# Kernel tuning notes

Hardware: AMD Instinct MI355X
Metric: run time of the kernel (lower is better)

Reference implementation:

```python
import jax, jax.numpy as jnp
import numpy as np

HIDDEN = 96
INF = 1e30


def setup_inputs() -> dict:
    key = jax.random.key(0)
    ks = jax.random.split(key, 9)
    B, JX, JM, D_IN, D_MEM = 8, 2048, 2048, 150, 150
    GATED = D_IN + D_MEM  # 300
    inputs = jax.random.normal(ks[0], (B, JX, D_IN), dtype=jnp.float32)
    memory = jax.random.normal(ks[1], (B, JM, D_MEM), dtype=jnp.float32)
    mask = jax.random.randint(ks[2], (B, JM), 0, 2, dtype=jnp.int32)
    s_in = 1.0 / np.sqrt(D_IN)
    s_g = 1.0 / np.sqrt(GATED)
    Wi = jax.random.uniform(ks[3], (D_IN, HIDDEN), jnp.float32, -s_in, s_in)
    bi = jax.random.uniform(ks[4], (HIDDEN,), jnp.float32, -s_in, s_in)
    Wm = jax.random.uniform(ks[5], (D_MEM, HIDDEN), jnp.float32, -s_in, s_in)
    bm = jax.random.uniform(ks[6], (HIDDEN,), jnp.float32, -s_in, s_in)
    Wg = jax.random.uniform(ks[7], (GATED, GATED), jnp.float32, -s_g, s_g)
    bg = jax.random.uniform(ks[8], (GATED,), jnp.float32, -s_g, s_g)
    return {"inputs": inputs, "memory": memory, "mask": mask,
            "Wi": Wi, "bi": bi, "Wm": Wm, "bm": bm, "Wg": Wg, "bg": bg}


def reference(inputs, memory, mask, Wi, bi, Wm, bm, Wg, bg):
    # ReLU projections (inference mode: dropout is identity)
    inputs_ = jax.nn.relu(jnp.einsum('bxd,dh->bxh', inputs, Wi) + bi)  # [B,JX,H]
    memory_ = jax.nn.relu(jnp.einsum('byd,dh->byh', memory, Wm) + bm)  # [B,JM,H]
    # Scaled dot-product scores [B,JX,JM]
    scores = jnp.einsum('bxh,byh->bxy', inputs_, memory_) / jnp.sqrt(
        jnp.asarray(HIDDEN, inputs.dtype))
    # Additive mask: -INF where mask==0 (broadcast over JX)
    maskf = mask.astype(inputs.dtype)[:, None, :]  # [B,1,JM]
    scores = scores - INF * (1.0 - maskf)
    logits = jax.nn.softmax(scores, axis=-1)
    outputs = jnp.einsum('bxy,byd->bxd', logits, memory)  # [B,JX,D_MEM]
    res = jnp.concatenate([inputs, outputs], axis=2)  # [B,JX,GATED]
    gate = jax.nn.sigmoid(jnp.einsum('bxg,gk->bxk', res, Wg) + bg)
    return gate * res
```

## Files before the change

### kernel.cpp

```cpp
#include <hip/hip_runtime.h>

#define BB 8
#define JX 2048
#define JMDIM 2048
#define DID 150
#define HID 96
#define GATED 300
#define NSPLIT 4

typedef unsigned short u16;
typedef __attribute__((ext_vector_type(8))) short bh8;
typedef __attribute__((ext_vector_type(4))) float f32x4;

#define M_INIT    (-3.0e38f)
#define SCALE2    (0.14724444f)
#define MASK_NEG2 (-1.4426950e30f)

__device__ inline float b2f(u16 u) {
    union { unsigned int i; float f; } c; c.i = ((unsigned int)u) << 16; return c.f;
}
__device__ inline u16 f2b(float f) {
    unsigned int u = __float_as_uint(f);
    unsigned int r = (u + 0x7fffu + ((u >> 16) & 1u)) >> 16;
    return (u16)r;
}

__global__ void prep_kernel(const float* __restrict__ Wi, const float* __restrict__ Wm,
                            const float* __restrict__ Wg,
                            u16* __restrict__ Wti, u16* __restrict__ Wtm,
                            u16* __restrict__ Wgt) {
    int tid = blockIdx.x * blockDim.x + threadIdx.x;
    int nthr = gridDim.x * blockDim.x;
    for (int e = tid; e < 96 * 168; e += nthr) {
        int h = e / 168, d = e - h * 168;
        Wti[e] = (d < DID) ? f2b(Wi[d * HID + h]) : (u16)0;
        Wtm[e] = (d < DID) ? f2b(Wm[d * HID + h]) : (u16)0;
    }
    for (int e = tid; e < 304 * 328; e += nthr) {
        int k = e / 328, d = e - k * 328;
        Wgt[e] = (k < GATED && d < GATED) ? f2b(Wg[d * GATED + k]) : (u16)0;
    }
}

__global__ __launch_bounds__(256) void proj2_kernel(
    const float* __restrict__ inputs, const float* __restrict__ memory,
    const u16* __restrict__ Wti, const u16* __restrict__ Wtm,
    const float* __restrict__ bi, const float* __restrict__ bm,
    u16* __restrict__ Qp, u16* __restrict__ Kp,
    u16* __restrict__ Xi, u16* __restrict__ Vt) {
    __shared__ __align__(16) u16 Xl[64 * 168];
    __shared__ __align__(16) u16 Wl[96 * 168];
    const float *X, *bias; const u16* Wt; u16* Y;
    if (blockIdx.y == 0) { X = inputs; Wt = Wti; bias = bi; Y = Qp; }
    else                 { X = memory; Wt = Wtm; bias = bm; Y = Kp; }
    int tid = threadIdx.x;
    size_t row0 = (size_t)blockIdx.x * 64;

    const float4* Xv = (const float4*)(X + row0 * DID);
    for (int i = tid; i < 2400; i += 256) {
        float4 v = Xv[i];
        int base = i * 4;
#pragma unroll
        for (int k = 0; k < 4; ++k) {
            int idx = base + k;
            int r = idx / DID, d = idx - r * DID;
            Xl[r * 168 + d] = f2b(((const float*)&v)[k]);
        }
    }
    for (int e = tid; e < 64 * 18; e += 256) {
        int r = e / 18, d = 150 + (e - r * 18);
        Xl[r * 168 + d] = 0;
    }
    for (int i = tid; i < 96 * 21; i += 256) {
        *(bh8*)(Wl + i * 8) = *(const bh8*)(Wt + i * 8);
    }
    __syncthreads();

    if (blockIdx.y == 0) {
        for (int e = tid; e < 64 * 20; e += 256) {
            int r = e / 20, c = e - r * 20;
            *(bh8*)(Xi + (row0 + r) * 160 + c * 8) = *(const bh8*)(Xl + r * 168 + c * 8);
        }
    } else {
        int b = blockIdx.x >> 5, jm0 = (blockIdx.x & 31) * 64;
        for (int e = tid; e < 160 * 64; e += 256) {
            int d = e >> 6, c = e & 63;
            Vt[((size_t)b * 160 + d) * JMDIM + jm0 + c] = Xl[c * 168 + d];
        }
    }

    int wave = tid >> 6, lane = tid & 63, quad = lane >> 4, l15 = lane & 15;
    bh8 af[5];
#pragma unroll
    for (int kc = 0; kc < 5; ++kc)
        af[kc] = *(const bh8*)(Xl + (wave * 16 + l15) * 168 + kc * 32 + quad * 8);
#pragma unroll
    for (int nt = 0; nt < 6; ++nt) {
        f32x4 acc = {0.f, 0.f, 0.f, 0.f};
#pragma unroll
        for (int kc = 0; kc < 5; ++kc) {
            bh8 bf = *(const bh8*)(Wl + (nt * 16 + l15) * 168 + kc * 32 + quad * 8);
            acc = __builtin_amdgcn_mfma_f32_16x16x32_bf16(af[kc], bf, acc, 0, 0, 0);
        }
        int h = nt * 16 + l15;
        float bv = bias[h];
#pragma unroll
        for (int j = 0; j < 4; ++j) {
            float y = acc[j] + bv;
            y = y > 0.f ? y : 0.f;
            Y[(row0 + wave * 16 + quad * 4 + j) * HID + h] = f2b(y);
        }
    }
}

template <int SPLIT>
__global__ __launch_bounds__(256, 3) void attn_kernel(
    const u16* __restrict__ Qp, const u16* __restrict__ Kp,
    const u16* __restrict__ Vt, const int* __restrict__ mask,
    u16* __restrict__ O, float* __restrict__ Opart,
    float* __restrict__ mpart, float* __restrict__ lpart) {
    __shared__ __align__(16) u16 KP[64 * 104];
    __shared__ __align__(16) u16 Vl[160 * 72];
    __shared__ float Ml[64];
    const int b = blockIdx.y;
    const int x0 = blockIdx.x * 64;
    const int tid = threadIdx.x;
    const int wave = tid >> 6, lane = tid & 63;
    const int quad = lane >> 4, l15 = lane & 15;

    bh8 qf[3];
    const u16* qbase = Qp + ((size_t)b * JX + x0 + wave * 16 + l15) * HID + quad * 8;
    qf[0] = *(const bh8*)(qbase);
    qf[1] = *(const bh8*)(qbase + 32);
    qf[2] = *(const bh8*)(qbase + 64);

    f32x4 o[10];
    const f32x4 zero4 = {0.f, 0.f, 0.f, 0.f};
#pragma unroll
    for (int i = 0; i < 10; ++i) o[i] = zero4;
    float m_r[4] = {M_INIT, M_INIT, M_INIT, M_INIT};
    float l_r[4] = {0.f, 0.f, 0.f, 0.f};

    const int nIter = 32 / SPLIT;
    const int jm0_0 = blockIdx.z * nIter * 64;

    const u16* kptr[3]; u16* kdst[3];
#pragma unroll
    for (int t = 0; t < 3; ++t) {
        int i = tid + t * 256, r = i / 12, c = i - r * 12;
        kptr[t] = Kp + ((size_t)b * JMDIM + jm0_0 + r) * HID + c * 8;
        kdst[t] = KP + r * 104 + c * 8;
    }
    const u16* vptr[5]; u16* vdst[5];
#pragma unroll
    for (int t = 0; t < 5; ++t) {
        int i = tid + t * 256, d = i >> 3, c = i & 7;
        vptr[t] = Vt + ((size_t)b * 160 + d) * JMDIM + jm0_0 + c * 8;
        vdst[t] = Vl + d * 72 + c * 8;
    }
    const int* mptr = mask + b * JMDIM + jm0_0 + (tid & 63);

    bh8 kreg[3], vreg[5]; int mreg = 0;
#pragma unroll
    for (int t = 0; t < 3; ++t) { kreg[t] = *(const bh8*)kptr[t]; kptr[t] += 64 * HID; }
#pragma unroll
    for (int t = 0; t < 5; ++t) { vreg[t] = *(const bh8*)vptr[t]; vptr[t] += 64; }
    if (tid < 64) { mreg = *mptr; mptr += 64; }

    for (int it = 0; it < nIter; ++it) {
        __syncthreads();
#pragma unroll
        for (int t = 0; t < 3; ++t) *(bh8*)kdst[t] = kreg[t];
#pragma unroll
        for (int t = 0; t < 5; ++t) *(bh8*)vdst[t] = vreg[t];
        if (tid < 64) Ml[tid] = mreg ? 0.f : MASK_NEG2;
        if (it + 1 < nIter) {
#pragma unroll
            for (int t = 0; t < 3; ++t) { kreg[t] = *(const bh8*)kptr[t]; kptr[t] += 64 * HID; }
#pragma unroll
            for (int t = 0; t < 5; ++t) { vreg[t] = *(const bh8*)vptr[t]; vptr[t] += 64; }
            if (tid < 64) { mreg = *mptr; mptr += 64; }
        }
        __syncthreads();

        f32x4 s[4];
#pragma unroll
        for (int nt = 0; nt < 4; ++nt) {
            s[nt] = zero4;
#pragma unroll
            for (int kc = 0; kc < 3; ++kc) {
                bh8 bf = *(const bh8*)(KP + (nt * 16 + l15) * 104 + kc * 32 + quad * 8);
                s[nt] = __builtin_amdgcn_mfma_f32_16x16x32_bf16(qf[kc], bf, s[nt], 0, 0, 0);
            }
        }
        float mx[4] = {M_INIT, M_INIT, M_INIT, M_INIT};
#pragma unroll
        for (int nt = 0; nt < 4; ++nt) {
            float madd = Ml[nt * 16 + l15];
#pragma unroll
            for (int j = 0; j < 4; ++j) {
                s[nt][j] = s[nt][j] * SCALE2 + madd;
                mx[j] = fmaxf(mx[j], s[nt][j]);
            }
        }
#pragma unroll
        for (int off = 1; off < 16; off <<= 1)
#pragma unroll
            for (int j = 0; j < 4; ++j) mx[j] = fmaxf(mx[j], __shfl_xor(mx[j], off, 64));

        float al[4], rs[4];
#pragma unroll
        for (int j = 0; j < 4; ++j) {
            float mn = fmaxf(m_r[j], mx[j]);
            al[j] = exp2f(m_r[j] - mn);
            m_r[j] = mn;
            rs[j] = 0.f;
        }
        __syncthreads();

#pragma unroll
        for (int nt = 0; nt < 4; ++nt)
#pragma unroll
            for (int j = 0; j < 4; ++j) {
                float p = exp2f(s[nt][j] - m_r[j]);
                rs[j] += p;
                KP[(wave * 16 + quad * 4 + j) * 72 + nt * 16 + l15] = f2b(p);
            }
#pragma unroll
        for (int off = 1; off < 16; off <<= 1)
#pragma unroll
            for (int j = 0; j < 4; ++j) rs[j] += __shfl_xor(rs[j], off, 64);
#pragma unroll
        for (int j = 0; j < 4; ++j) l_r[j] = l_r[j] * al[j] + rs[j];
        if (al[0] + al[1] + al[2] + al[3] < 4.0f) {
#pragma unroll
            for (int nt = 0; nt < 10; ++nt)
#pragma unroll
                for (int j = 0; j < 4; ++j) o[nt][j] *= al[j];
        }
        __threadfence_block();

        bh8 pf[2];
        pf[0] = *(const bh8*)(KP + (wave * 16 + l15) * 72 + quad * 8);
        pf[1] = *(const bh8*)(KP + (wave * 16 + l15) * 72 + 32 + quad * 8);
#pragma unroll
        for (int nt = 0; nt < 10; ++nt) {
#pragma unroll
            for (int kc = 0; kc < 2; ++kc) {
                bh8 bf = *(const bh8*)(Vl + (nt * 16 + l15) * 72 + kc * 32 + quad * 8);
                o[nt] = __builtin_amdgcn_mfma_f32_16x16x32_bf16(pf[kc], bf, o[nt], 0, 0, 0);
            }
        }
    }

    if (SPLIT == 1) {
        float inv[4];
#pragma unroll
        for (int j = 0; j < 4; ++j) inv[j] = 1.f / l_r[j];
        size_t obase = ((size_t)b * JX + x0 + wave * 16) * 152;
#pragma unroll
        for (int nt = 0; nt < 10; ++nt) {
            int d = nt * 16 + l15;
            if (d < DID) {
#pragma unroll
                for (int j = 0; j < 4; ++j)
                    O[obase + (quad * 4 + j) * 152 + d] = f2b(o[nt][j] * inv[j]);
            }
        }
    } else {
        const int blk = b * (JX / 64) + blockIdx.x;
        const size_t pbase = ((size_t)blockIdx.z * 256 + blk) * 64 + wave * 16;
#pragma unroll
        for (int nt = 0; nt < 10; ++nt) {
            int d = nt * 16 + l15;
            if (d < 152) {
#pragma unroll
                for (int j = 0; j < 4; ++j)
                    Opart[(pbase + quad * 4 + j) * 152 + d] = o[nt][j];
            }
        }
        if (l15 == 0) {
#pragma unroll
            for (int j = 0; j < 4; ++j) {
                mpart[pbase + quad * 4 + j] = m_r[j];
                lpart[pbase + quad * 4 + j] = l_r[j];
            }
        }
    }
}

template <int SPLIT>
__global__ __launch_bounds__(256) void gate_kernel(
    const u16* __restrict__ Xi, const u16* __restrict__ Ow,
    const float* __restrict__ Opart, const float* __restrict__ mpart,
    const float* __restrict__ lpart,
    const u16* __restrict__ Wgt, const float* __restrict__ bg,
    float* __restrict__ out) {
    __shared__ __align__(16) u16 Rl[16 * 328];
    __shared__ float Cw[NSPLIT * 16];
    int tid = threadIdx.x;
    size_t row0 = (size_t)blockIdx.x * 16;
    const int ablk = blockIdx.x >> 2;
    const int rloc0 = (blockIdx.x & 3) * 16;

    if (SPLIT > 1 && tid < 16) {
        float m[NSPLIT], l[NSPLIT], M = M_INIT;
#pragma unroll
        for (int s = 0; s < NSPLIT; ++s) {
            m[s] = mpart[((size_t)s * 256 + ablk) * 64 + rloc0 + tid];
            l[s] = lpart[((size_t)s * 256 + ablk) * 64 + rloc0 + tid];
            M = fmaxf(M, m[s]);
        }
        float L = 0.f;
#pragma unroll
        for (int s = 0; s < NSPLIT; ++s) L += l[s] * exp2f(m[s] - M);
        float invL = 1.f / L;
#pragma unroll
        for (int s = 0; s < NSPLIT; ++s) Cw[s * 16 + tid] = exp2f(m[s] - M) * invL;
    }
    for (int e = tid; e < 16 * 20; e += 256) {
        int r = e / 20, c = e - r * 20;
        *(bh8*)(Rl + r * 328 + c * 8) = *(const bh8*)(Xi + (row0 + r) * 160 + c * 8);
    }
    __syncthreads();
    if (SPLIT > 1) {
        for (int e = tid; e < 16 * 38; e += 256) {
            int r = e / 38, q = e - r * 38;
            float a0 = 0.f, a1 = 0.f, a2 = 0.f, a3 = 0.f;
#pragma unroll
            for (int s = 0; s < NSPLIT; ++s) {
                const float4 v = *(const float4*)(Opart +
                    (((size_t)s * 256 + ablk) * 64 + rloc0 + r) * 152 + q * 4);
                float w = Cw[s * 16 + r];
                a0 += v.x * w; a1 += v.y * w; a2 += v.z * w; a3 += v.w * w;
            }
            u16* dst = Rl + r * 328 + 150 + q * 4;
            dst[0] = f2b(a0); dst[1] = f2b(a1); dst[2] = f2b(a2); dst[3] = f2b(a3);
        }
    } else {
        for (int e = tid; e < 16 * 152; e += 256) {
            int r = e / 152, dd = e - r * 152;
            Rl[r * 328 + 150 + dd] = (dd < DID) ? Ow[(row0 + r) * 152 + dd] : (u16)0;
        }
    }
    for (int e = tid; e < 16 * 26; e += 256) {
        int r = e / 26, c = 302 + (e - r * 26);
        Rl[r * 328 + c] = 0;
    }
    __syncthreads();

    int wave = tid >> 6, lane = tid & 63, quad = lane >> 4, l15 = lane & 15;
    bh8 af[10];
#pragma unroll
    for (int kc = 0; kc < 10; ++kc)
        af[kc] = *(const bh8*)(Rl + l15 * 328 + kc * 32 + quad * 8);
    for (int nt = wave; nt < 19; nt += 4) {
        int h = nt * 16 + l15;
        f32x4 acc = {0.f, 0.f, 0.f, 0.f};
#pragma unroll
        for (int kc = 0; kc < 10; ++kc) {
            bh8 bf = *(const bh8*)(Wgt + (size_t)h * 328 + kc * 32 + quad * 8);
            acc = __builtin_amdgcn_mfma_f32_16x16x32_bf16(af[kc], bf, acc, 0, 0, 0);
        }
        if (h < GATED) {
            float bv = bg[h];
#pragma unroll
            for (int j = 0; j < 4; ++j) {
                int r = quad * 4 + j;
                float x = acc[j] + bv;
                float g = 1.f / (1.f + __expf(-x));
                float rv = b2f(Rl[r * 328 + h]);
                out[(row0 + r) * GATED + h] = g * rv;
            }
        }
    }
}

extern "C" void kernel_launch(void* const* d_in, const int* in_sizes, int n_in,
                              void* d_out, int out_size, void* d_ws, size_t ws_size,
                              hipStream_t stream) {
    const float* inputs = (const float*)d_in[0];
    const float* memory = (const float*)d_in[1];
    const int*   mask   = (const int*)d_in[2];
    const float* Wi = (const float*)d_in[3];
    const float* bi = (const float*)d_in[4];
    const float* Wm = (const float*)d_in[5];
    const float* bm = (const float*)d_in[6];
    const float* Wg = (const float*)d_in[7];
    const float* bg = (const float*)d_in[8];
    float* out = (float*)d_out;

    u16* Qp  = (u16*)d_ws;
    u16* Kp  = Qp + (size_t)BB * JX * HID;
    u16* Vt  = Kp + (size_t)BB * JMDIM * HID;
    u16* Xi  = Vt + (size_t)BB * 160 * JMDIM;
    u16* Ow  = Xi + (size_t)BB * JX * 160;
    u16* Wti = Ow + (size_t)BB * JX * 152;
    u16* Wtm = Wti + 96 * 168;
    u16* Wgt = Wtm + 96 * 168;
    size_t u16_elems = (size_t)(Wgt - Qp) + 304 * 328;
    size_t base_bytes = ((u16_elems * sizeof(u16)) + 15) & ~(size_t)15;
    float* Opart = (float*)((char*)d_ws + base_bytes);
    float* mpart = Opart + (size_t)NSPLIT * 256 * 64 * 152;
    float* lpart = mpart + (size_t)NSPLIT * 256 * 64;
    size_t split_bytes = base_bytes +
        ((size_t)NSPLIT * 256 * 64 * 152 + 2 * (size_t)NSPLIT * 256 * 64) * 4;
    if (ws_size < u16_elems * sizeof(u16)) return;
    bool use_split = (ws_size >= split_bytes);

    prep_kernel<<<dim3(128), 256, 0, stream>>>(Wi, Wm, Wg, Wti, Wtm, Wgt);
    proj2_kernel<<<dim3(BB * JX / 64, 2), 256, 0, stream>>>(
        inputs, memory, Wti, Wtm, bi, bm, Qp, Kp, Xi, Vt);
    if (use_split) {
        attn_kernel<NSPLIT><<<dim3(JX / 64, BB, NSPLIT), 256, 0, stream>>>(
            Qp, Kp, Vt, mask, Ow, Opart, mpart, lpart);
        gate_kernel<NSPLIT><<<dim3(BB * JX / 16), 256, 0, stream>>>(
            Xi, Ow, Opart, mpart, lpart, Wgt, bg, out);
    } else {
        attn_kernel<1><<<dim3(JX / 64, BB, 1), 256, 0, stream>>>(
            Qp, Kp, Vt, mask, Ow, Opart, mpart, lpart);
        gate_kernel<1><<<dim3(BB * JX / 16), 256, 0, stream>>>(
            Xi, Ow, Opart, mpart, lpart, Wgt, bg, out);
    }
}
```

Baseline: 171.6 us.

## Process two query tiles per wave and store normalized split partials in bf16

Each attention block now covers 128 query rows, with every wave handling two 16-row tiles. Each K and V fragment loaded from LDS therefore feeds two MFMAs, which halves LDS traffic per unit of work and amortizes K/V staging. P gets its own LDS buffer, so one barrier is dropped. Split partial outputs are normalized per split and stored as bf16 instead of fp32, roughly halving the partial-sum traffic between attention and the gate kernel, and the non-split fallback path is removed. The cost is more registers (occupancy hint lowered to 2), half as many attention blocks (512), and extra bf16 rounding in the partials.

```diff
diff --git a/kernel.cpp b/kernel.cpp
--- a/kernel.cpp
+++ b/kernel.cpp
@@ -7,6 +7,7 @@
 #define HID 96
 #define GATED 300
 #define NSPLIT 4
+#define NROWS (BB * JX)
 
 typedef unsigned short u16;
 typedef __attribute__((ext_vector_type(8))) short bh8;
@@ -114,32 +115,41 @@
 }
 
 template <int SPLIT>
-__global__ __launch_bounds__(256, 3) void attn_kernel(
+__global__ __launch_bounds__(256, 2) void attn_kernel(
     const u16* __restrict__ Qp, const u16* __restrict__ Kp,
     const u16* __restrict__ Vt, const int* __restrict__ mask,
-    u16* __restrict__ O, float* __restrict__ Opart,
-    float* __restrict__ mpart, float* __restrict__ lpart) {
-    __shared__ __align__(16) u16 KP[64 * 104];
+    u16* __restrict__ Opart, float* __restrict__ mpart,
+    float* __restrict__ lpart) {
+    __shared__ __align__(16) u16 Kl[64 * 104];
     __shared__ __align__(16) u16 Vl[160 * 72];
+    __shared__ __align__(16) u16 Pl[128 * 72];
     __shared__ float Ml[64];
     const int b = blockIdx.y;
-    const int x0 = blockIdx.x * 64;
+    const int x0 = blockIdx.x * 128;
     const int tid = threadIdx.x;
     const int wave = tid >> 6, lane = tid & 63;
     const int quad = lane >> 4, l15 = lane & 15;
 
-    bh8 qf[3];
-    const u16* qbase = Qp + ((size_t)b * JX + x0 + wave * 16 + l15) * HID + quad * 8;
-    qf[0] = *(const bh8*)(qbase);
-    qf[1] = *(const bh8*)(qbase + 32);
-    qf[2] = *(const bh8*)(qbase + 64);
-
-    f32x4 o[10];
+    bh8 qf[2][3];
+#pragma unroll
+    for (int mt = 0; mt < 2; ++mt) {
+        const u16* qb = Qp + ((size_t)b * JX + x0 + wave * 32 + mt * 16 + l15) * HID + quad * 8;
+        qf[mt][0] = *(const bh8*)(qb);
+        qf[mt][1] = *(const bh8*)(qb + 32);
+        qf[mt][2] = *(const bh8*)(qb + 64);
+    }
+
+    f32x4 o[2][10];
     const f32x4 zero4 = {0.f, 0.f, 0.f, 0.f};
 #pragma unroll
-    for (int i = 0; i < 10; ++i) o[i] = zero4;
-    float m_r[4] = {M_INIT, M_INIT, M_INIT, M_INIT};
-    float l_r[4] = {0.f, 0.f, 0.f, 0.f};
+    for (int mt = 0; mt < 2; ++mt)
+#pragma unroll
+        for (int i = 0; i < 10; ++i) o[mt][i] = zero4;
+    float m_r[2][4], l_r[2][4];
+#pragma unroll
+    for (int mt = 0; mt < 2; ++mt)
+#pragma unroll
+        for (int j = 0; j < 4; ++j) { m_r[mt][j] = M_INIT; l_r[mt][j] = 0.f; }
 
     const int nIter = 32 / SPLIT;
     const int jm0_0 = blockIdx.z * nIter * 64;
@@ -149,7 +159,7 @@
     for (int t = 0; t < 3; ++t) {
         int i = tid + t * 256, r = i / 12, c = i - r * 12;
         kptr[t] = Kp + ((size_t)b * JMDIM + jm0_0 + r) * HID + c * 8;
-        kdst[t] = KP + r * 104 + c * 8;
+        kdst[t] = Kl + r * 104 + c * 8;
     }
     const u16* vptr[5]; u16* vdst[5];
 #pragma unroll
@@ -183,107 +193,110 @@
         }
         __syncthreads();
 
-        f32x4 s[4];
+        f32x4 s[2][4];
+#pragma unroll
+        for (int mt = 0; mt < 2; ++mt)
+#pragma unroll
+            for (int nt = 0; nt < 4; ++nt) s[mt][nt] = zero4;
 #pragma unroll
         for (int nt = 0; nt < 4; ++nt) {
-            s[nt] = zero4;
 #pragma unroll
             for (int kc = 0; kc < 3; ++kc) {
-                bh8 bf = *(const bh8*)(KP + (nt * 16 + l15) * 104 + kc * 32 + quad * 8);
-                s[nt] = __builtin_amdgcn_mfma_f32_16x16x32_bf16(qf[kc], bf, s[nt], 0, 0, 0);
-            }
-        }
-        float mx[4] = {M_INIT, M_INIT, M_INIT, M_INIT};
-#pragma unroll
-        for (int nt = 0; nt < 4; ++nt) {
-            float madd = Ml[nt * 16 + l15];
+                bh8 bf = *(const bh8*)(Kl + (nt * 16 + l15) * 104 + kc * 32 + quad * 8);
+                s[0][nt] = __builtin_amdgcn_mfma_f32_16x16x32_bf16(qf[0][kc], bf, s[0][nt], 0, 0, 0);
+                s[1][nt] = __builtin_amdgcn_mfma_f32_16x16x32_bf16(qf[1][kc], bf, s[1][nt], 0, 0, 0);
+            }
+        }
+        float alsum = 0.f;
+#pragma unroll
+        for (int mt = 0; mt < 2; ++mt) {
+            float mx[4] = {M_INIT, M_INIT, M_INIT, M_INIT};
+#pragma unroll
+            for (int nt = 0; nt < 4; ++nt) {
+                float madd = Ml[nt * 16 + l15];
+#pragma unroll
+                for (int j = 0; j < 4; ++j) {
+                    s[mt][nt][j] = s[mt][nt][j] * SCALE2 + madd;
+                    mx[j] = fmaxf(mx[j], s[mt][nt][j]);
+                }
+            }
+#pragma unroll
+            for (int off = 1; off < 16; off <<= 1)
+#pragma unroll
+                for (int j = 0; j < 4; ++j) mx[j] = fmaxf(mx[j], __shfl_xor(mx[j], off, 64));
+            float al[4], rs[4];
 #pragma unroll
             for (int j = 0; j < 4; ++j) {
-                s[nt][j] = s[nt][j] * SCALE2 + madd;
-                mx[j] = fmaxf(mx[j], s[nt][j]);
-            }
-        }
-#pragma unroll
-        for (int off = 1; off < 16; off <<= 1)
-#pragma unroll
-            for (int j = 0; j < 4; ++j) mx[j] = fmaxf(mx[j], __shfl_xor(mx[j], off, 64));
-
-        float al[4], rs[4];
-#pragma unroll
-        for (int j = 0; j < 4; ++j) {
-            float mn = fmaxf(m_r[j], mx[j]);
-            al[j] = exp2f(m_r[j] - mn);
-            m_r[j] = mn;
-            rs[j] = 0.f;
-        }
-        __syncthreads();
-
-#pragma unroll
-        for (int nt = 0; nt < 4; ++nt)
+                float mn = fmaxf(m_r[mt][j], mx[j]);
+                al[j] = exp2f(m_r[mt][j] - mn);
+                m_r[mt][j] = mn;
+                rs[j] = 0.f;
+            }
+#pragma unroll
+            for (int nt = 0; nt < 4; ++nt)
+#pragma unroll
+                for (int j = 0; j < 4; ++j) {
+                    float p = exp2f(s[mt][nt][j] - m_r[mt][j]);
+                    rs[j] += p;
+                    Pl[(wave * 32 + mt * 16 + quad * 4 + j) * 72 + nt * 16 + l15] = f2b(p);
+                }
+#pragma unroll
+            for (int off = 1; off < 16; off <<= 1)
+#pragma unroll
+                for (int j = 0; j < 4; ++j) rs[j] += __shfl_xor(rs[j], off, 64);
 #pragma unroll
             for (int j = 0; j < 4; ++j) {
-                float p = exp2f(s[nt][j] - m_r[j]);
-                rs[j] += p;
-                KP[(wave * 16 + quad * 4 + j) * 72 + nt * 16 + l15] = f2b(p);
-            }
-#pragma unroll
-        for (int off = 1; off < 16; off <<= 1)
-#pragma unroll
-            for (int j = 0; j < 4; ++j) rs[j] += __shfl_xor(rs[j], off, 64);
-#pragma unroll
-        for (int j = 0; j < 4; ++j) l_r[j] = l_r[j] * al[j] + rs[j];
-        if (al[0] + al[1] + al[2] + al[3] < 4.0f) {
-#pragma unroll
-            for (int nt = 0; nt < 10; ++nt)
-#pragma unroll
-                for (int j = 0; j < 4; ++j) o[nt][j] *= al[j];
-        }
+                l_r[mt][j] = l_r[mt][j] * al[j] + rs[j];
+                alsum += al[j];
+            }
+            if (al[0] + al[1] + al[2] + al[3] < 4.0f) {
+#pragma unroll
+                for (int nt = 0; nt < 10; ++nt)
+#pragma unroll
+                    for (int j = 0; j < 4; ++j) o[mt][nt][j] *= al[j];
+            }
+        }
+        (void)alsum;
         __threadfence_block();
 
-        bh8 pf[2];
-        pf[0] = *(const bh8*)(KP + (wave * 16 + l15) * 72 + quad * 8);
-        pf[1] = *(const bh8*)(KP + (wave * 16 + l15) * 72 + 32 + quad * 8);
+        bh8 pf[2][2];
+#pragma unroll
+        for (int mt = 0; mt < 2; ++mt) {
+            pf[mt][0] = *(const bh8*)(Pl + (wave * 32 + mt * 16 + l15) * 72 + quad * 8);
+            pf[mt][1] = *(const bh8*)(Pl + (wave * 32 + mt * 16 + l15) * 72 + 32 + quad * 8);
+        }
 #pragma unroll
         for (int nt = 0; nt < 10; ++nt) {
 #pragma unroll
             for (int kc = 0; kc < 2; ++kc) {
                 bh8 bf = *(const bh8*)(Vl + (nt * 16 + l15) * 72 + kc * 32 + quad * 8);
-                o[nt] = __builtin_amdgcn_mfma_f32_16x16x32_bf16(pf[kc], bf, o[nt], 0, 0, 0);
-            }
-        }
-    }
-
-    if (SPLIT == 1) {
+                o[0][nt] = __builtin_amdgcn_mfma_f32_16x16x32_bf16(pf[0][kc], bf, o[0][nt], 0, 0, 0);
+                o[1][nt] = __builtin_amdgcn_mfma_f32_16x16x32_bf16(pf[1][kc], bf, o[1][nt], 0, 0, 0);
+            }
+        }
+    }
+
+    const size_t z = blockIdx.z;
+#pragma unroll
+    for (int mt = 0; mt < 2; ++mt) {
         float inv[4];
 #pragma unroll
-        for (int j = 0; j < 4; ++j) inv[j] = 1.f / l_r[j];
-        size_t obase = ((size_t)b * JX + x0 + wave * 16) * 152;
-#pragma unroll
-        for (int nt = 0; nt < 10; ++nt) {
-            int d = nt * 16 + l15;
-            if (d < DID) {
-#pragma unroll
-                for (int j = 0; j < 4; ++j)
-                    O[obase + (quad * 4 + j) * 152 + d] = f2b(o[nt][j] * inv[j]);
-            }
-        }
-    } else {
-        const int blk = b * (JX / 64) + blockIdx.x;
-        const size_t pbase = ((size_t)blockIdx.z * 256 + blk) * 64 + wave * 16;
+        for (int j = 0; j < 4; ++j) inv[j] = (l_r[mt][j] > 0.f) ? 1.f / l_r[mt][j] : 0.f;
+        size_t grow = (size_t)b * JX + x0 + wave * 32 + mt * 16;
 #pragma unroll
         for (int nt = 0; nt < 10; ++nt) {
             int d = nt * 16 + l15;
             if (d < 152) {
 #pragma unroll
                 for (int j = 0; j < 4; ++j)
-                    Opart[(pbase + quad * 4 + j) * 152 + d] = o[nt][j];
+                    Opart[(z * NROWS + grow + quad * 4 + j) * 152 + d] = f2b(o[mt][nt][j] * inv[j]);
             }
         }
         if (l15 == 0) {
 #pragma unroll
             for (int j = 0; j < 4; ++j) {
-                mpart[pbase + quad * 4 + j] = m_r[j];
-                lpart[pbase + quad * 4 + j] = l_r[j];
+                mpart[z * NROWS + grow + quad * 4 + j] = m_r[mt][j];
+                lpart[z * NROWS + grow + quad * 4 + j] = l_r[mt][j];
             }
         }
     }
@@ -291,57 +304,51 @@
 
 template <int SPLIT>
 __global__ __launch_bounds__(256) void gate_kernel(
-    const u16* __restrict__ Xi, const u16* __restrict__ Ow,
-    const float* __restrict__ Opart, const float* __restrict__ mpart,
-    const float* __restrict__ lpart,
+    const u16* __restrict__ Xi, const u16* __restrict__ Opart,
+    const float* __restrict__ mpart, const float* __restrict__ lpart,
     const u16* __restrict__ Wgt, const float* __restrict__ bg,
     float* __restrict__ out) {
     __shared__ __align__(16) u16 Rl[16 * 328];
-    __shared__ float Cw[NSPLIT * 16];
+    __shared__ float Cw[SPLIT * 16];
     int tid = threadIdx.x;
     size_t row0 = (size_t)blockIdx.x * 16;
-    const int ablk = blockIdx.x >> 2;
-    const int rloc0 = (blockIdx.x & 3) * 16;
-
-    if (SPLIT > 1 && tid < 16) {
-        float m[NSPLIT], l[NSPLIT], M = M_INIT;
-#pragma unroll
-        for (int s = 0; s < NSPLIT; ++s) {
-            m[s] = mpart[((size_t)s * 256 + ablk) * 64 + rloc0 + tid];
-            l[s] = lpart[((size_t)s * 256 + ablk) * 64 + rloc0 + tid];
+
+    if (tid < 16) {
+        float m[SPLIT], l[SPLIT], M = M_INIT;
+#pragma unroll
+        for (int s = 0; s < SPLIT; ++s) {
+            m[s] = mpart[(size_t)s * NROWS + row0 + tid];
+            l[s] = lpart[(size_t)s * NROWS + row0 + tid];
             M = fmaxf(M, m[s]);
         }
         float L = 0.f;
 #pragma unroll
-        for (int s = 0; s < NSPLIT; ++s) L += l[s] * exp2f(m[s] - M);
-        float invL = 1.f / L;
-#pragma unroll
-        for (int s = 0; s < NSPLIT; ++s) Cw[s * 16 + tid] = exp2f(m[s] - M) * invL;
+        for (int s = 0; s < SPLIT; ++s) L += l[s] * exp2f(m[s] - M);
+        float invL = (L > 0.f) ? 1.f / L : 0.f;
+#pragma unroll
+        for (int s = 0; s < SPLIT; ++s)
+            Cw[s * 16 + tid] = l[s] * exp2f(m[s] - M) * invL;
     }
     for (int e = tid; e < 16 * 20; e += 256) {
         int r = e / 20, c = e - r * 20;
         *(bh8*)(Rl + r * 328 + c * 8) = *(const bh8*)(Xi + (row0 + r) * 160 + c * 8);
     }
     __syncthreads();
-    if (SPLIT > 1) {
-        for (int e = tid; e < 16 * 38; e += 256) {
-            int r = e / 38, q = e - r * 38;
-            float a0 = 0.f, a1 = 0.f, a2 = 0.f, a3 = 0.f;
-#pragma unroll
-            for (int s = 0; s < NSPLIT; ++s) {
-                const float4 v = *(const float4*)(Opart +
-                    (((size_t)s * 256 + ablk) * 64 + rloc0 + r) * 152 + q * 4);
-                float w = Cw[s * 16 + r];
-                a0 += v.x * w; a1 += v.y * w; a2 += v.z * w; a3 += v.w * w;
-            }
-            u16* dst = Rl + r * 328 + 150 + q * 4;
-            dst[0] = f2b(a0); dst[1] = f2b(a1); dst[2] = f2b(a2); dst[3] = f2b(a3);
-        }
-    } else {
-        for (int e = tid; e < 16 * 152; e += 256) {
-            int r = e / 152, dd = e - r * 152;
-            Rl[r * 328 + 150 + dd] = (dd < DID) ? Ow[(row0 + r) * 152 + dd] : (u16)0;
-        }
+    for (int e = tid; e < 16 * 19; e += 256) {
+        int r = e / 19, q = e - r * 19;
+        float acc[8];
+#pragma unroll
+        for (int k = 0; k < 8; ++k) acc[k] = 0.f;
+#pragma unroll
+        for (int s = 0; s < SPLIT; ++s) {
+            bh8 v = *(const bh8*)(Opart + ((size_t)s * NROWS + row0 + r) * 152 + q * 8);
+            float w = Cw[s * 16 + r];
+#pragma unroll
+            for (int k = 0; k < 8; ++k) acc[k] += b2f(((const u16*)&v)[k]) * w;
+        }
+        u16* dst = Rl + r * 328 + 150 + q * 8;
+#pragma unroll
+        for (int k = 0; k < 8; ++k) dst[k] = f2b(acc[k]);
     }
     for (int e = tid; e < 16 * 26; e += 256) {
         int r = e / 26, c = 302 + (e - r * 26);
@@ -391,35 +398,25 @@
     float* out = (float*)d_out;
 
     u16* Qp  = (u16*)d_ws;
-    u16* Kp  = Qp + (size_t)BB * JX * HID;
-    u16* Vt  = Kp + (size_t)BB * JMDIM * HID;
+    u16* Kp  = Qp + (size_t)NROWS * HID;
+    u16* Vt  = Kp + (size_t)NROWS * HID;
     u16* Xi  = Vt + (size_t)BB * 160 * JMDIM;
-    u16* Ow  = Xi + (size_t)BB * JX * 160;
-    u16* Wti = Ow + (size_t)BB * JX * 152;
+    u16* Wti = Xi + (size_t)NROWS * 160;
     u16* Wtm = Wti + 96 * 168;
     u16* Wgt = Wtm + 96 * 168;
-    size_t u16_elems = (size_t)(Wgt - Qp) + 304 * 328;
+    u16* Opart = Wgt + 304 * 328;
+    size_t u16_elems = (size_t)(Opart - Qp) + (size_t)NSPLIT * NROWS * 152;
     size_t base_bytes = ((u16_elems * sizeof(u16)) + 15) & ~(size_t)15;
-    float* Opart = (float*)((char*)d_ws + base_bytes);
-    float* mpart = Opart + (size_t)NSPLIT * 256 * 64 * 152;
-    float* lpart = mpart + (size_t)NSPLIT * 256 * 64;
-    size_t split_bytes = base_bytes +
-        ((size_t)NSPLIT * 256 * 64 * 152 + 2 * (size_t)NSPLIT * 256 * 64) * 4;
-    if (ws_size < u16_elems * sizeof(u16)) return;
-    bool use_split = (ws_size >= split_bytes);
+    float* mpart = (float*)((char*)d_ws + base_bytes);
+    float* lpart = mpart + (size_t)NSPLIT * NROWS;
+    size_t needed = base_bytes + 2 * (size_t)NSPLIT * NROWS * sizeof(float);
+    if (ws_size < needed) return;
 
     prep_kernel<<<dim3(128), 256, 0, stream>>>(Wi, Wm, Wg, Wti, Wtm, Wgt);
-    proj2_kernel<<<dim3(BB * JX / 64, 2), 256, 0, stream>>>(
+    proj2_kernel<<<dim3(NROWS / 64, 2), 256, 0, stream>>>(
         inputs, memory, Wti, Wtm, bi, bm, Qp, Kp, Xi, Vt);
-    if (use_split) {
-        attn_kernel<NSPLIT><<<dim3(JX / 64, BB, NSPLIT), 256, 0, stream>>>(
-            Qp, Kp, Vt, mask, Ow, Opart, mpart, lpart);
-        gate_kernel<NSPLIT><<<dim3(BB * JX / 16), 256, 0, stream>>>(
-            Xi, Ow, Opart, mpart, lpart, Wgt, bg, out);
-    } else {
-        attn_kernel<1><<<dim3(JX / 64, BB, 1), 256, 0, stream>>>(
-            Qp, Kp, Vt, mask, Ow, Opart, mpart, lpart);
-        gate_kernel<1><<<dim3(BB * JX / 16), 256, 0, stream>>>(
-            Xi, Ow, Opart, mpart, lpart, Wgt, bg, out);
-    }
-}
+    attn_kernel<NSPLIT><<<dim3(JX / 128, BB, NSPLIT), 256, 0, stream>>>(
+        Qp, Kp, Vt, mask, Opart, mpart, lpart);
+    gate_kernel<NSPLIT><<<dim3(NROWS / 16), 256, 0, stream>>>(
+        Xi, Opart, mpart, lpart, Wgt, bg, out);
+}
```

Result: faster. 159.1 us (-7.3%).
